# Kernel optimization log

Hardware: AMD Instinct MI355X
Metric: run time of the kernel (lower is better)

## Reference

```python
import jax, jax.numpy as jnp
import numpy as np

GROUP_SIZE = 128
TOP_K = 2
ZERO_POINT = 8  # Marlin symmetric zero point: w = scale * (q - 8)


def _dequant_int4(q, scales, group_size):
    # q: [E, N, K] int values in [0,15]; scales: [E, N, K//group_size]
    s = jnp.repeat(scales, group_size, axis=-1)  # [E, N, K]
    return (q.astype(jnp.float32) - float(ZERO_POINT)) * s


def setup_inputs() -> dict:
    key = jax.random.key(0)
    k1, k2, k3, k4, k5, k6 = jax.random.split(key, 6)
    B, S, H, I, E = 2, 1024, 2048, 1408, 8
    router_logits = jax.random.normal(k1, (B, S, E), dtype=jnp.float32)
    hidden_states = jax.random.normal(k2, (B, S, H), dtype=jnp.float32)
    fc_gate_up_qweights = jax.random.randint(k3, (E, 2 * I, H), 0, 16, dtype=jnp.int32)
    fc_gate_up_scales = jax.random.uniform(k4, (E, 2 * I, H // GROUP_SIZE), dtype=jnp.float32) * 0.02
    fc_down_qweights = jax.random.randint(k5, (E, H, I), 0, 16, dtype=jnp.int32)
    fc_down_scales = jax.random.uniform(k6, (E, H, I // GROUP_SIZE), dtype=jnp.float32) * 0.02
    return {
        "router_logits": router_logits,
        "hidden_states": hidden_states,
        "fc_gate_up_qweights": fc_gate_up_qweights,
        "fc_gate_up_scales": fc_gate_up_scales,
        "fc_down_qweights": fc_down_qweights,
        "fc_down_scales": fc_down_scales,
    }


def reference(router_logits, hidden_states, fc_gate_up_qweights, fc_gate_up_scales,
              fc_down_qweights, fc_down_scales):
    B, S, H = hidden_states.shape
    E = router_logits.shape[-1]
    T = B * S
    x = hidden_states.reshape(T, H)
    logits = router_logits.reshape(T, E)

    # top-k routing with softmax over selected logits
    top_vals, top_idx = jax.lax.top_k(logits, TOP_K)          # [T, k]
    top_w = jax.nn.softmax(top_vals, axis=-1)                 # [T, k]
    route_w = jnp.zeros((T, E), x.dtype).at[jnp.arange(T)[:, None], top_idx].set(top_w)  # [T, E]

    # dequantize int4 weights: scale * (q - 8), per-group along K
    w_gate_up = _dequant_int4(fc_gate_up_qweights, fc_gate_up_scales, GROUP_SIZE)  # [E, 2I, H]
    w_down = _dequant_int4(fc_down_qweights, fc_down_scales, GROUP_SIZE)          # [E, H, I]

    # grouped GEMM (dense over experts, masked by routing weights)
    gu = jnp.einsum('th,enh->ten', x, w_gate_up)              # [T, E, 2I]
    gate, up = jnp.split(gu, 2, axis=-1)
    act = jax.nn.silu(gate) * up                              # SwiGLU, [T, E, I]
    out = jnp.einsum('tei,ehi,te->th', act, w_down, route_w)  # [T, H]
    return out.reshape(B, S, H)
```

## Files before the change

kernel.cpp:

```cpp
#include <hip/hip_runtime.h>
#include <hip/hip_bf16.h>

#define T_TOKENS 2048
#define H_DIM    2048
#define I_DIM    1408
#define E_NUM    8

typedef __bf16 bf16;
typedef __attribute__((ext_vector_type(8))) __bf16  bf16x8;
typedef __attribute__((ext_vector_type(4))) float   floatx4;

static const size_t OFF_COUNTS = 0;
static const size_t OFF_LISTS  = 256;
static const size_t OFF_WLISTS = OFF_LISTS + (size_t)T_TOKENS * E_NUM * 4;
static const size_t OFF_XB     = 131328;
static const size_t OFF_ACT    = OFF_XB + (size_t)T_TOKENS * H_DIM * 2;
static const size_t OFF_GUPK   = OFF_ACT + (size_t)2 * T_TOKENS * I_DIM * 2;
static const size_t OFF_DNPK   = OFF_GUPK + (size_t)E_NUM * 22 * 32 * 16384;
static const size_t OFF_TMP    = OFF_GUPK;

__device__ __forceinline__ void gload_lds16(const bf16* g, bf16* l)
{
    __builtin_amdgcn_global_load_lds((const __attribute__((address_space(1))) void*)g,
                                     (__attribute__((address_space(3))) void*)l,
                                     16, 0, 0);
}

__global__ __launch_bounds__(256) void prep_kernel(
    const int*   __restrict__ gu_q,
    const float* __restrict__ gu_s,
    bf16*        __restrict__ gu_pk,
    const float* __restrict__ x,
    bf16*        __restrict__ xb,
    const float* __restrict__ logits,
    int*         __restrict__ counts,
    int*         __restrict__ lists,
    float*       __restrict__ wlists)
{
    const int bid = blockIdx.x;
    const int tid = threadIdx.x;

    if (bid < 5632) {
        const int kt  = bid & 31;
        const int en  = bid >> 5;
        const int nt  = en % 22;
        const int e   = en / 22;
        bf16x8* ob = reinterpret_cast<bf16x8*>(gu_pk) + (size_t)bid * 1024;
        #pragma unroll
        for (int j = 0; j < 4; ++j) {
            const int s     = tid + 256 * j;
            const int r     = s >> 3;
            const int gl    = (s & 7) ^ (r & 7);
            const int p2    = r >> 4;
            const int is_up = p2 & 1;
            const int icol  = nt * 64 + (p2 >> 1) * 16 + (r & 15);
            const size_t row_q = (size_t)e * 2816 + (is_up ? I_DIM : 0) + icol;
            const int4* qp = reinterpret_cast<const int4*>(gu_q + row_q * H_DIM + kt * 64 + gl * 8);
            int4 a = qp[0], c = qp[1];
            float sv = gu_s[row_q * 16 + (kt >> 1)];
            float m8 = -8.f * sv;
            bf16x8 bv;
            bv[0] = (bf16)fmaf((float)a.x, sv, m8);
            bv[1] = (bf16)fmaf((float)a.y, sv, m8);
            bv[2] = (bf16)fmaf((float)a.z, sv, m8);
            bv[3] = (bf16)fmaf((float)a.w, sv, m8);
            bv[4] = (bf16)fmaf((float)c.x, sv, m8);
            bv[5] = (bf16)fmaf((float)c.y, sv, m8);
            bv[6] = (bf16)fmaf((float)c.z, sv, m8);
            bv[7] = (bf16)fmaf((float)c.w, sv, m8);
            ob[s] = bv;
        }
    } else if (bid < 5632 + 2048) {
        const int i = (bid - 5632) * 256 + tid;
        const float4* x4 = reinterpret_cast<const float4*>(x) + (size_t)i * 2;
        float4 v0 = x4[0], v1 = x4[1];
        bf16x8 bv;
        bv[0] = (bf16)v0.x; bv[1] = (bf16)v0.y; bv[2] = (bf16)v0.z; bv[3] = (bf16)v0.w;
        bv[4] = (bf16)v1.x; bv[5] = (bf16)v1.y; bv[6] = (bf16)v1.z; bv[7] = (bf16)v1.w;
        *reinterpret_cast<bf16x8*>(xb + (size_t)i * 8) = bv;
    } else {
        const int t = (bid - 7680) * 256 + tid;
        const float* l = logits + (size_t)t * E_NUM;
        float v0 = -1e30f, v1 = -1e30f;
        int i0 = 0, i1 = 0;
        #pragma unroll
        for (int e = 0; e < E_NUM; ++e) {
            float v = l[e];
            if (v > v0) { v1 = v0; i1 = i0; v0 = v; i0 = e; }
            else if (v > v1) { v1 = v; i1 = e; }
        }
        float w0 = 1.f / (1.f + __expf(v1 - v0));
        float w1 = 1.f - w0;
        int p0 = atomicAdd(&counts[i0], 1);
        lists[i0 * T_TOKENS + p0] = t * 2 + 0;
        wlists[i0 * T_TOKENS + p0] = w0;
        int p1 = atomicAdd(&counts[i1], 1);
        lists[i1 * T_TOKENS + p1] = t * 2 + 1;
        wlists[i1 * T_TOKENS + p1] = w1;
    }
}

__global__ __launch_bounds__(256) void gemm1_packdn_kernel(
    const bf16*  __restrict__ xb,
    const bf16*  __restrict__ wpk,
    const int*   __restrict__ counts,
    const int*   __restrict__ lists,
    bf16*        __restrict__ act,
    const int*   __restrict__ dn_q,
    const float* __restrict__ dn_s,
    bf16*        __restrict__ dn_pk)
{
    const int tid = threadIdx.x;

    if (blockIdx.x >= 5632) {
        const int pbid = blockIdx.x - 5632;
        const int kt  = pbid % 22;
        const int en  = pbid / 22;
        const int nt  = en & 15;
        const int e   = en >> 4;
        bf16x8* ob = reinterpret_cast<bf16x8*>(dn_pk) + (size_t)pbid * 1024;
        #pragma unroll
        for (int j = 0; j < 4; ++j) {
            const int s  = tid + 256 * j;
            const int r  = s >> 3;
            const int gl = (s & 7) ^ (r & 7);
            const size_t row_q = (size_t)e * 2048 + nt * 128 + r;
            const int4* qp = reinterpret_cast<const int4*>(dn_q + row_q * I_DIM + kt * 64 + gl * 8);
            int4 a = qp[0], c = qp[1];
            float sv = dn_s[row_q * 11 + (kt >> 1)];
            float m8 = -8.f * sv;
            bf16x8 bv;
            bv[0] = (bf16)fmaf((float)a.x, sv, m8);
            bv[1] = (bf16)fmaf((float)a.y, sv, m8);
            bv[2] = (bf16)fmaf((float)a.z, sv, m8);
            bv[3] = (bf16)fmaf((float)a.w, sv, m8);
            bv[4] = (bf16)fmaf((float)c.x, sv, m8);
            bv[5] = (bf16)fmaf((float)c.y, sv, m8);
            bv[6] = (bf16)fmaf((float)c.z, sv, m8);
            bv[7] = (bf16)fmaf((float)c.w, sv, m8);
            ob[s] = bv;
        }
        return;
    }

    const int lid = (blockIdx.x & 7) * 704 + (blockIdx.x >> 3);
    const int e   = lid / 704;
    const int r_  = lid - e * 704;
    const int nt  = r_ >> 5;
    const int m0  = (r_ & 31) << 6;
    const int cnt = counts[e];
    if (m0 >= cnt) return;

    __shared__ __align__(16) bf16 Al[4096];
    __shared__ __align__(16) bf16 Bl[8192];
    __shared__ int meta[64];

    if (tid < 64) {
        int m = m0 + tid;
        meta[tid] = lists[e * T_TOKENS + (m < cnt ? m : 0)];
    }
    __syncthreads();

    const int lane = tid & 63;
    const int wv = tid >> 6;
    const int wm = wv >> 1, wn = wv & 1;

    size_t agbl[2];
    #pragma unroll
    for (int j = 0; j < 2; ++j) {
        int g = tid + 256 * j;
        int arow = g >> 3, cg = g & 7;
        agbl[j] = (size_t)(meta[arow] >> 1) * H_DIM + ((cg ^ (arow & 7)) * 8);
    }
    const bf16* bt = wpk + ((size_t)e * 22 + nt) * (32 * 8192) + tid * 8;

    int afr[2][2], bfr[2][4];
    #pragma unroll
    for (int ks = 0; ks < 2; ++ks) {
        int gidx = ks * 4 + (lane >> 4);
        #pragma unroll
        for (int t4 = 0; t4 < 2; ++t4) {
            int ra = wm * 32 + t4 * 16 + (lane & 15);
            afr[ks][t4] = ra * 64 + ((gidx ^ (ra & 7)) * 8);
        }
        #pragma unroll
        for (int t4 = 0; t4 < 4; ++t4) {
            int rb = wn * 64 + t4 * 16 + (lane & 15);
            bfr[ks][t4] = rb * 64 + ((gidx ^ (rb & 7)) * 8);
        }
    }

    floatx4 acc[2][4];
    #pragma unroll
    for (int i = 0; i < 2; ++i)
        #pragma unroll
        for (int j = 0; j < 4; ++j)
            acc[i][j] = (floatx4){0.f, 0.f, 0.f, 0.f};

    for (int k0 = 0; k0 < H_DIM; k0 += 64) {
        #pragma unroll
        for (int j = 0; j < 2; ++j)
            gload_lds16(xb + agbl[j] + k0, &Al[(tid + 256 * j) * 8]);
        const bf16* bsrc = bt + (size_t)(k0 >> 6) * 8192;
        #pragma unroll
        for (int j = 0; j < 4; ++j)
            gload_lds16(bsrc + j * 2048, &Bl[tid * 8 + j * 2048]);
        __syncthreads();
        #pragma unroll
        for (int ks = 0; ks < 2; ++ks) {
            bf16x8 af[2], bff[4];
            #pragma unroll
            for (int mt = 0; mt < 2; ++mt)
                af[mt] = *reinterpret_cast<const bf16x8*>(&Al[afr[ks][mt]]);
            #pragma unroll
            for (int ntf = 0; ntf < 4; ++ntf)
                bff[ntf] = *reinterpret_cast<const bf16x8*>(&Bl[bfr[ks][ntf]]);
            #pragma unroll
            for (int mt = 0; mt < 2; ++mt)
                #pragma unroll
                for (int ntf = 0; ntf < 4; ++ntf)
                    acc[mt][ntf] = __builtin_amdgcn_mfma_f32_16x16x32_bf16(af[mt], bff[ntf], acc[mt][ntf], 0, 0, 0);
        }
        __syncthreads();
    }

    const int rbase = (lane >> 4) * 4;
    const int cn = lane & 15;
    #pragma unroll
    for (int mt = 0; mt < 2; ++mt) {
        #pragma unroll
        for (int j = 0; j < 2; ++j) {
            floatx4 g = acc[mt][2 * j];
            floatx4 u = acc[mt][2 * j + 1];
            int col = nt * 64 + (wn * 2 + j) * 16 + cn;
            #pragma unroll
            for (int r = 0; r < 4; ++r) {
                int lrow = wm * 32 + mt * 16 + rbase + r;
                if (m0 + lrow < cnt) {
                    float gate = g[r], up = u[r];
                    float a = gate / (1.f + __expf(-gate)) * up;
                    act[(size_t)meta[lrow] * I_DIM + col] = (bf16)a;
                }
            }
        }
    }
}

__global__ __launch_bounds__(256) void gemm2_kernel(
    const bf16*  __restrict__ act,
    const bf16*  __restrict__ wpk,
    const int*   __restrict__ counts,
    const int*   __restrict__ lists,
    const float* __restrict__ wlists,
    float*       __restrict__ tmp)
{
    const int lid = (blockIdx.x & 7) * 512 + (blockIdx.x >> 3);
    const int e   = lid >> 9;
    const int r_  = lid & 511;
    const int nt  = r_ >> 5;
    const int m0  = (r_ & 31) << 6;
    const int cnt = counts[e];
    if (m0 >= cnt) return;

    __shared__ __align__(16) bf16 Al[4096];
    __shared__ __align__(16) bf16 Bl[8192];
    __shared__ int   meta[64];
    __shared__ float wmeta[64];

    const int tid = threadIdx.x;
    if (tid < 64) {
        int m = m0 + tid;
        int mm = (m < cnt) ? m : 0;
        meta[tid]  = lists[e * T_TOKENS + mm];
        wmeta[tid] = wlists[e * T_TOKENS + mm];
    }
    __syncthreads();

    const int lane = tid & 63;
    const int wv = tid >> 6;
    const int wm = wv >> 1, wn = wv & 1;

    size_t agbl[2];
    #pragma unroll
    for (int j = 0; j < 2; ++j) {
        int g = tid + 256 * j;
        int arow = g >> 3, cg = g & 7;
        agbl[j] = (size_t)meta[arow] * I_DIM + ((cg ^ (arow & 7)) * 8);
    }
    const bf16* bt = wpk + ((size_t)e * 16 + nt) * (22 * 8192) + tid * 8;

    int afr[2][2], bfr[2][4];
    #pragma unroll
    for (int ks = 0; ks < 2; ++ks) {
        int gidx = ks * 4 + (lane >> 4);
        #pragma unroll
        for (int t4 = 0; t4 < 2; ++t4) {
            int ra = wm * 32 + t4 * 16 + (lane & 15);
            afr[ks][t4] = ra * 64 + ((gidx ^ (ra & 7)) * 8);
        }
        #pragma unroll
        for (int t4 = 0; t4 < 4; ++t4) {
            int rb = wn * 64 + t4 * 16 + (lane & 15);
            bfr[ks][t4] = rb * 64 + ((gidx ^ (rb & 7)) * 8);
        }
    }

    floatx4 acc[2][4];
    #pragma unroll
    for (int i = 0; i < 2; ++i)
        #pragma unroll
        for (int j = 0; j < 4; ++j)
            acc[i][j] = (floatx4){0.f, 0.f, 0.f, 0.f};

    for (int kt = 0; kt < 22; ++kt) {
        #pragma unroll
        for (int j = 0; j < 2; ++j)
            gload_lds16(act + agbl[j] + kt * 64, &Al[(tid + 256 * j) * 8]);
        const bf16* bsrc = bt + (size_t)kt * 8192;
        #pragma unroll
        for (int j = 0; j < 4; ++j)
            gload_lds16(bsrc + j * 2048, &Bl[tid * 8 + j * 2048]);
        __syncthreads();
        #pragma unroll
        for (int ks = 0; ks < 2; ++ks) {
            bf16x8 af[2], bff[4];
            #pragma unroll
            for (int mt = 0; mt < 2; ++mt)
                af[mt] = *reinterpret_cast<const bf16x8*>(&Al[afr[ks][mt]]);
            #pragma unroll
            for (int ntf = 0; ntf < 4; ++ntf)
                bff[ntf] = *reinterpret_cast<const bf16x8*>(&Bl[bfr[ks][ntf]]);
            #pragma unroll
            for (int mt = 0; mt < 2; ++mt)
                #pragma unroll
                for (int ntf = 0; ntf < 4; ++ntf)
                    acc[mt][ntf] = __builtin_amdgcn_mfma_f32_16x16x32_bf16(af[mt], bff[ntf], acc[mt][ntf], 0, 0, 0);
        }
        __syncthreads();
    }

    const int rbase = (lane >> 4) * 4;
    const int cn = lane & 15;
    #pragma unroll
    for (int mt = 0; mt < 2; ++mt) {
        #pragma unroll
        for (int ntf = 0; ntf < 4; ++ntf) {
            floatx4 v = acc[mt][ntf];
            int col = nt * 128 + wn * 64 + ntf * 16 + cn;
            #pragma unroll
            for (int r = 0; r < 4; ++r) {
                int lrow = wm * 32 + mt * 16 + rbase + r;
                if (m0 + lrow < cnt) {
                    tmp[(size_t)meta[lrow] * H_DIM + col] = wmeta[lrow] * v[r];
                }
            }
        }
    }
}

__global__ void finalize_kernel(const float* __restrict__ tmp, float* __restrict__ out)
{
    int i4 = blockIdx.x * blockDim.x + threadIdx.x;
    int t  = i4 >> 9;
    int h  = (i4 & 511) * 4;
    float4 a = *reinterpret_cast<const float4*>(tmp + ((size_t)2 * t) * H_DIM + h);
    float4 b = *reinterpret_cast<const float4*>(tmp + ((size_t)(2 * t + 1)) * H_DIM + h);
    float4 o;
    o.x = a.x + b.x; o.y = a.y + b.y; o.z = a.z + b.z; o.w = a.w + b.w;
    *reinterpret_cast<float4*>(out + (size_t)t * H_DIM + h) = o;
}

extern "C" void kernel_launch(void* const* d_in, const int* in_sizes, int n_in,
                              void* d_out, int out_size, void* d_ws, size_t ws_size,
                              hipStream_t stream)
{
    const float* router_logits = (const float*)d_in[0];
    const float* x             = (const float*)d_in[1];
    const int*   gu_q          = (const int*)d_in[2];
    const float* gu_s          = (const float*)d_in[3];
    const int*   dn_q          = (const int*)d_in[4];
    const float* dn_s          = (const float*)d_in[5];
    float* out = (float*)d_out;

    char* ws = (char*)d_ws;
    int*   counts = (int*)(ws + OFF_COUNTS);
    int*   lists  = (int*)(ws + OFF_LISTS);
    float* wlists = (float*)(ws + OFF_WLISTS);
    bf16*  xb     = (bf16*)(ws + OFF_XB);
    bf16*  act    = (bf16*)(ws + OFF_ACT);
    bf16*  gu_pk  = (bf16*)(ws + OFF_GUPK);
    bf16*  dn_pk  = (bf16*)(ws + OFF_DNPK);
    float* tmp    = (float*)(ws + OFF_TMP);

    hipMemsetAsync(counts, 0, E_NUM * sizeof(int), stream);

    prep_kernel<<<7688, 256, 0, stream>>>(gu_q, gu_s, gu_pk, x, xb,
                                          router_logits, counts, lists, wlists);
    gemm1_packdn_kernel<<<8448, 256, 0, stream>>>(xb, gu_pk, counts, lists, act,
                                                  dn_q, dn_s, dn_pk);
    gemm2_kernel<<<4096, 256, 0, stream>>>(act, dn_pk, counts, lists, wlists, tmp);
    finalize_kernel<<<4096, 256, 0, stream>>>(tmp, out);
}
```

Baseline: 489.0 us.

## Load A operand fragments directly from global memory instead of staging in LDS

Both grouped GEMM kernels drop the LDS staging buffer for the gathered activation (A) tile and have each lane load its MFMA A fragment straight from global memory via per-row base pointers. This removes the A-side LDS writes and reads and halves the LDS footprint, which may allow higher occupancy. In exchange, each A element is now read from global/L2 by both N-waves (wn=0,1) instead of once per block, and the loads are issued after the barrier inside the compute loop, so their latency is exposed right before the MFMAs.

```diff
diff --git a/kernel.cpp b/kernel.cpp
--- a/kernel.cpp
+++ b/kernel.cpp
@@ -151,7 +151,6 @@
     const int cnt = counts[e];
     if (m0 >= cnt) return;
 
-    __shared__ __align__(16) bf16 Al[4096];
     __shared__ __align__(16) bf16 Bl[8192];
     __shared__ int meta[64];
 
@@ -165,24 +164,19 @@
     const int wv = tid >> 6;
     const int wm = wv >> 1, wn = wv & 1;
 
-    size_t agbl[2];
-    #pragma unroll
-    for (int j = 0; j < 2; ++j) {
-        int g = tid + 256 * j;
-        int arow = g >> 3, cg = g & 7;
-        agbl[j] = (size_t)(meta[arow] >> 1) * H_DIM + ((cg ^ (arow & 7)) * 8);
-    }
+    const bf16* abase[2];
+    #pragma unroll
+    for (int mt = 0; mt < 2; ++mt) {
+        int ra = wm * 32 + mt * 16 + (lane & 15);
+        abase[mt] = xb + (size_t)(meta[ra] >> 1) * H_DIM + ((lane >> 4) * 8);
+    }
+
     const bf16* bt = wpk + ((size_t)e * 22 + nt) * (32 * 8192) + tid * 8;
 
-    int afr[2][2], bfr[2][4];
+    int bfr[2][4];
     #pragma unroll
     for (int ks = 0; ks < 2; ++ks) {
         int gidx = ks * 4 + (lane >> 4);
-        #pragma unroll
-        for (int t4 = 0; t4 < 2; ++t4) {
-            int ra = wm * 32 + t4 * 16 + (lane & 15);
-            afr[ks][t4] = ra * 64 + ((gidx ^ (ra & 7)) * 8);
-        }
         #pragma unroll
         for (int t4 = 0; t4 < 4; ++t4) {
             int rb = wn * 64 + t4 * 16 + (lane & 15);
@@ -198,9 +192,6 @@
             acc[i][j] = (floatx4){0.f, 0.f, 0.f, 0.f};
 
     for (int k0 = 0; k0 < H_DIM; k0 += 64) {
-        #pragma unroll
-        for (int j = 0; j < 2; ++j)
-            gload_lds16(xb + agbl[j] + k0, &Al[(tid + 256 * j) * 8]);
         const bf16* bsrc = bt + (size_t)(k0 >> 6) * 8192;
         #pragma unroll
         for (int j = 0; j < 4; ++j)
@@ -211,7 +202,7 @@
             bf16x8 af[2], bff[4];
             #pragma unroll
             for (int mt = 0; mt < 2; ++mt)
-                af[mt] = *reinterpret_cast<const bf16x8*>(&Al[afr[ks][mt]]);
+                af[mt] = *reinterpret_cast<const bf16x8*>(abase[mt] + k0 + ks * 32);
             #pragma unroll
             for (int ntf = 0; ntf < 4; ++ntf)
                 bff[ntf] = *reinterpret_cast<const bf16x8*>(&Bl[bfr[ks][ntf]]);
@@ -262,7 +253,6 @@
     const int cnt = counts[e];
     if (m0 >= cnt) return;
 
-    __shared__ __align__(16) bf16 Al[4096];
     __shared__ __align__(16) bf16 Bl[8192];
     __shared__ int   meta[64];
     __shared__ float wmeta[64];
@@ -280,24 +270,19 @@
     const int wv = tid >> 6;
     const int wm = wv >> 1, wn = wv & 1;
 
-    size_t agbl[2];
-    #pragma unroll
-    for (int j = 0; j < 2; ++j) {
-        int g = tid + 256 * j;
-        int arow = g >> 3, cg = g & 7;
-        agbl[j] = (size_t)meta[arow] * I_DIM + ((cg ^ (arow & 7)) * 8);
-    }
+    const bf16* abase[2];
+    #pragma unroll
+    for (int mt = 0; mt < 2; ++mt) {
+        int ra = wm * 32 + mt * 16 + (lane & 15);
+        abase[mt] = act + (size_t)meta[ra] * I_DIM + ((lane >> 4) * 8);
+    }
+
     const bf16* bt = wpk + ((size_t)e * 16 + nt) * (22 * 8192) + tid * 8;
 
-    int afr[2][2], bfr[2][4];
+    int bfr[2][4];
     #pragma unroll
     for (int ks = 0; ks < 2; ++ks) {
         int gidx = ks * 4 + (lane >> 4);
-        #pragma unroll
-        for (int t4 = 0; t4 < 2; ++t4) {
-            int ra = wm * 32 + t4 * 16 + (lane & 15);
-            afr[ks][t4] = ra * 64 + ((gidx ^ (ra & 7)) * 8);
-        }
         #pragma unroll
         for (int t4 = 0; t4 < 4; ++t4) {
             int rb = wn * 64 + t4 * 16 + (lane & 15);
@@ -313,9 +298,6 @@
             acc[i][j] = (floatx4){0.f, 0.f, 0.f, 0.f};
 
     for (int kt = 0; kt < 22; ++kt) {
-        #pragma unroll
-        for (int j = 0; j < 2; ++j)
-            gload_lds16(act + agbl[j] + kt * 64, &Al[(tid + 256 * j) * 8]);
         const bf16* bsrc = bt + (size_t)kt * 8192;
         #pragma unroll
         for (int j = 0; j < 4; ++j)
@@ -326,7 +308,7 @@
             bf16x8 af[2], bff[4];
             #pragma unroll
             for (int mt = 0; mt < 2; ++mt)
-                af[mt] = *reinterpret_cast<const bf16x8*>(&Al[afr[ks][mt]]);
+                af[mt] = *reinterpret_cast<const bf16x8*>(abase[mt] + kt * 64 + ks * 32);
             #pragma unroll
             for (int ntf = 0; ntf < 4; ++ntf)
                 bff[ntf] = *reinterpret_cast<const bf16x8*>(&Bl[bfr[ks][ntf]]);
```

After: 605.9 us. 1.24x slower.

## Double-buffer LDS tiles in both MoE GEMMs with async prefetch

Applied to the files above, without the earlier changes.

Both grouped GEMM kernels now use two LDS buffers for the A and B tiles and issue global-to-LDS loads for the next K tile before computing on the current one. Partial vmcnt waits plus raw barriers with sched_barrier replace __syncthreads, so the wait covers only the current tile's loads. This aims to hide global memory latency behind MFMA work. In exchange it doubles LDS usage per block, which may lower occupancy, and it relies on a hand-written vmcnt count.

```diff
diff --git a/kernel.cpp b/kernel.cpp
--- a/kernel.cpp
+++ b/kernel.cpp
@@ -25,6 +25,10 @@
                                      (__attribute__((address_space(3))) void*)l,
                                      16, 0, 0);
 }
+
+#define RAW_BAR() do { __builtin_amdgcn_sched_barrier(0); \
+                       __builtin_amdgcn_s_barrier(); \
+                       __builtin_amdgcn_sched_barrier(0); } while (0)
 
 __global__ __launch_bounds__(256) void prep_kernel(
     const int*   __restrict__ gu_q,
@@ -151,8 +155,8 @@
     const int cnt = counts[e];
     if (m0 >= cnt) return;
 
-    __shared__ __align__(16) bf16 Al[4096];
-    __shared__ __align__(16) bf16 Bl[8192];
+    __shared__ __align__(16) bf16 Al[2][4096];
+    __shared__ __align__(16) bf16 Bl[2][8192];
     __shared__ int meta[64];
 
     if (tid < 64) {
@@ -197,31 +201,46 @@
         for (int j = 0; j < 4; ++j)
             acc[i][j] = (floatx4){0.f, 0.f, 0.f, 0.f};
 
-    for (int k0 = 0; k0 < H_DIM; k0 += 64) {
-        #pragma unroll
-        for (int j = 0; j < 2; ++j)
-            gload_lds16(xb + agbl[j] + k0, &Al[(tid + 256 * j) * 8]);
-        const bf16* bsrc = bt + (size_t)(k0 >> 6) * 8192;
-        #pragma unroll
-        for (int j = 0; j < 4; ++j)
-            gload_lds16(bsrc + j * 2048, &Bl[tid * 8 + j * 2048]);
-        __syncthreads();
+    #pragma unroll
+    for (int j = 0; j < 2; ++j)
+        gload_lds16(xb + agbl[j], &Al[0][(tid + 256 * j) * 8]);
+    #pragma unroll
+    for (int j = 0; j < 4; ++j)
+        gload_lds16(bt + j * 2048, &Bl[0][tid * 8 + j * 2048]);
+
+    for (int kt = 0; kt < 32; ++kt) {
+        const int cur = kt & 1;
+        if (kt < 31) {
+            const int k1 = (kt + 1) * 64;
+            #pragma unroll
+            for (int j = 0; j < 2; ++j)
+                gload_lds16(xb + agbl[j] + k1, &Al[cur ^ 1][(tid + 256 * j) * 8]);
+            const bf16* bsrc = bt + (size_t)(kt + 1) * 8192;
+            #pragma unroll
+            for (int j = 0; j < 4; ++j)
+                gload_lds16(bsrc + j * 2048, &Bl[cur ^ 1][tid * 8 + j * 2048]);
+            asm volatile("s_waitcnt vmcnt(6)" ::: "memory");
+        } else {
+            asm volatile("s_waitcnt vmcnt(0)" ::: "memory");
+        }
+        RAW_BAR();
+
         #pragma unroll
         for (int ks = 0; ks < 2; ++ks) {
             bf16x8 af[2], bff[4];
             #pragma unroll
             for (int mt = 0; mt < 2; ++mt)
-                af[mt] = *reinterpret_cast<const bf16x8*>(&Al[afr[ks][mt]]);
+                af[mt] = *reinterpret_cast<const bf16x8*>(&Al[cur][afr[ks][mt]]);
             #pragma unroll
             for (int ntf = 0; ntf < 4; ++ntf)
-                bff[ntf] = *reinterpret_cast<const bf16x8*>(&Bl[bfr[ks][ntf]]);
+                bff[ntf] = *reinterpret_cast<const bf16x8*>(&Bl[cur][bfr[ks][ntf]]);
             #pragma unroll
             for (int mt = 0; mt < 2; ++mt)
                 #pragma unroll
                 for (int ntf = 0; ntf < 4; ++ntf)
                     acc[mt][ntf] = __builtin_amdgcn_mfma_f32_16x16x32_bf16(af[mt], bff[ntf], acc[mt][ntf], 0, 0, 0);
         }
-        __syncthreads();
+        RAW_BAR();
     }
 
     const int rbase = (lane >> 4) * 4;
@@ -262,8 +281,8 @@
     const int cnt = counts[e];
     if (m0 >= cnt) return;
 
-    __shared__ __align__(16) bf16 Al[4096];
-    __shared__ __align__(16) bf16 Bl[8192];
+    __shared__ __align__(16) bf16 Al[2][4096];
+    __shared__ __align__(16) bf16 Bl[2][8192];
     __shared__ int   meta[64];
     __shared__ float wmeta[64];
 
@@ -312,31 +331,46 @@
         for (int j = 0; j < 4; ++j)
             acc[i][j] = (floatx4){0.f, 0.f, 0.f, 0.f};
 
+    #pragma unroll
+    for (int j = 0; j < 2; ++j)
+        gload_lds16(act + agbl[j], &Al[0][(tid + 256 * j) * 8]);
+    #pragma unroll
+    for (int j = 0; j < 4; ++j)
+        gload_lds16(bt + j * 2048, &Bl[0][tid * 8 + j * 2048]);
+
     for (int kt = 0; kt < 22; ++kt) {
-        #pragma unroll
-        for (int j = 0; j < 2; ++j)
-            gload_lds16(act + agbl[j] + kt * 64, &Al[(tid + 256 * j) * 8]);
-        const bf16* bsrc = bt + (size_t)kt * 8192;
-        #pragma unroll
-        for (int j = 0; j < 4; ++j)
-            gload_lds16(bsrc + j * 2048, &Bl[tid * 8 + j * 2048]);
-        __syncthreads();
+        const int cur = kt & 1;
+        if (kt < 21) {
+            const int k1 = (kt + 1) * 64;
+            #pragma unroll
+            for (int j = 0; j < 2; ++j)
+                gload_lds16(act + agbl[j] + k1, &Al[cur ^ 1][(tid + 256 * j) * 8]);
+            const bf16* bsrc = bt + (size_t)(kt + 1) * 8192;
+            #pragma unroll
+            for (int j = 0; j < 4; ++j)
+                gload_lds16(bsrc + j * 2048, &Bl[cur ^ 1][tid * 8 + j * 2048]);
+            asm volatile("s_waitcnt vmcnt(6)" ::: "memory");
+        } else {
+            asm volatile("s_waitcnt vmcnt(0)" ::: "memory");
+        }
+        RAW_BAR();
+
         #pragma unroll
         for (int ks = 0; ks < 2; ++ks) {
             bf16x8 af[2], bff[4];
             #pragma unroll
             for (int mt = 0; mt < 2; ++mt)
-                af[mt] = *reinterpret_cast<const bf16x8*>(&Al[afr[ks][mt]]);
+                af[mt] = *reinterpret_cast<const bf16x8*>(&Al[cur][afr[ks][mt]]);
             #pragma unroll
             for (int ntf = 0; ntf < 4; ++ntf)
-                bff[ntf] = *reinterpret_cast<const bf16x8*>(&Bl[bfr[ks][ntf]]);
+                bff[ntf] = *reinterpret_cast<const bf16x8*>(&Bl[cur][bfr[ks][ntf]]);
             #pragma unroll
             for (int mt = 0; mt < 2; ++mt)
                 #pragma unroll
                 for (int ntf = 0; ntf < 4; ++ntf)
                     acc[mt][ntf] = __builtin_amdgcn_mfma_f32_16x16x32_bf16(af[mt], bff[ntf], acc[mt][ntf], 0, 0, 0);
         }
-        __syncthreads();
+        RAW_BAR();
     }
 
     const int rbase = (lane >> 4) * 4;
```

New measurement: 511.6 us. 4.6% more time.

## Fuse int4 weight dequantization into GEMM tile loads, dropping the pre-pack passes

Applied to the files above, without the earlier changes.

Removes the separate passes that dequantized gate/up and down weights into packed bf16 buffers, and instead has each GEMM block read int32 quantized weights and scales directly, dequantize in registers, and store to LDS. This eliminates the pack writes and the workspace buffers. In exchange, every m-tile re-reads the 4-byte-per-element quantized weights and repeats the conversion math, and B loads become synchronous register loads instead of direct-to-LDS loads.

```diff
diff --git a/kernel.cpp b/kernel.cpp
--- a/kernel.cpp
+++ b/kernel.cpp
@@ -15,9 +15,7 @@
 static const size_t OFF_WLISTS = OFF_LISTS + (size_t)T_TOKENS * E_NUM * 4;
 static const size_t OFF_XB     = 131328;
 static const size_t OFF_ACT    = OFF_XB + (size_t)T_TOKENS * H_DIM * 2;
-static const size_t OFF_GUPK   = OFF_ACT + (size_t)2 * T_TOKENS * I_DIM * 2;
-static const size_t OFF_DNPK   = OFF_GUPK + (size_t)E_NUM * 22 * 32 * 16384;
-static const size_t OFF_TMP    = OFF_GUPK;
+static const size_t OFF_TMP    = OFF_ACT + (size_t)2 * T_TOKENS * I_DIM * 2;
 
 __device__ __forceinline__ void gload_lds16(const bf16* g, bf16* l)
 {
@@ -27,9 +25,6 @@
 }
 
 __global__ __launch_bounds__(256) void prep_kernel(
-    const int*   __restrict__ gu_q,
-    const float* __restrict__ gu_s,
-    bf16*        __restrict__ gu_pk,
     const float* __restrict__ x,
     bf16*        __restrict__ xb,
     const float* __restrict__ logits,
@@ -40,38 +35,8 @@
     const int bid = blockIdx.x;
     const int tid = threadIdx.x;
 
-    if (bid < 5632) {
-        const int kt  = bid & 31;
-        const int en  = bid >> 5;
-        const int nt  = en % 22;
-        const int e   = en / 22;
-        bf16x8* ob = reinterpret_cast<bf16x8*>(gu_pk) + (size_t)bid * 1024;
-        #pragma unroll
-        for (int j = 0; j < 4; ++j) {
-            const int s     = tid + 256 * j;
-            const int r     = s >> 3;
-            const int gl    = (s & 7) ^ (r & 7);
-            const int p2    = r >> 4;
-            const int is_up = p2 & 1;
-            const int icol  = nt * 64 + (p2 >> 1) * 16 + (r & 15);
-            const size_t row_q = (size_t)e * 2816 + (is_up ? I_DIM : 0) + icol;
-            const int4* qp = reinterpret_cast<const int4*>(gu_q + row_q * H_DIM + kt * 64 + gl * 8);
-            int4 a = qp[0], c = qp[1];
-            float sv = gu_s[row_q * 16 + (kt >> 1)];
-            float m8 = -8.f * sv;
-            bf16x8 bv;
-            bv[0] = (bf16)fmaf((float)a.x, sv, m8);
-            bv[1] = (bf16)fmaf((float)a.y, sv, m8);
-            bv[2] = (bf16)fmaf((float)a.z, sv, m8);
-            bv[3] = (bf16)fmaf((float)a.w, sv, m8);
-            bv[4] = (bf16)fmaf((float)c.x, sv, m8);
-            bv[5] = (bf16)fmaf((float)c.y, sv, m8);
-            bv[6] = (bf16)fmaf((float)c.z, sv, m8);
-            bv[7] = (bf16)fmaf((float)c.w, sv, m8);
-            ob[s] = bv;
-        }
-    } else if (bid < 5632 + 2048) {
-        const int i = (bid - 5632) * 256 + tid;
+    if (bid < 2048) {
+        const int i = bid * 256 + tid;
         const float4* x4 = reinterpret_cast<const float4*>(x) + (size_t)i * 2;
         float4 v0 = x4[0], v1 = x4[1];
         bf16x8 bv;
@@ -79,7 +44,7 @@
         bv[4] = (bf16)v1.x; bv[5] = (bf16)v1.y; bv[6] = (bf16)v1.z; bv[7] = (bf16)v1.w;
         *reinterpret_cast<bf16x8*>(xb + (size_t)i * 8) = bv;
     } else {
-        const int t = (bid - 7680) * 256 + tid;
+        const int t = (bid - 2048) * 256 + tid;
         const float* l = logits + (size_t)t * E_NUM;
         float v0 = -1e30f, v1 = -1e30f;
         int i0 = 0, i1 = 0;
@@ -100,49 +65,14 @@
     }
 }
 
-__global__ __launch_bounds__(256) void gemm1_packdn_kernel(
+__global__ __launch_bounds__(256) void gemm1_kernel(
     const bf16*  __restrict__ xb,
-    const bf16*  __restrict__ wpk,
+    const int*   __restrict__ q,
+    const float* __restrict__ sc,
     const int*   __restrict__ counts,
     const int*   __restrict__ lists,
-    bf16*        __restrict__ act,
-    const int*   __restrict__ dn_q,
-    const float* __restrict__ dn_s,
-    bf16*        __restrict__ dn_pk)
-{
-    const int tid = threadIdx.x;
-
-    if (blockIdx.x >= 5632) {
-        const int pbid = blockIdx.x - 5632;
-        const int kt  = pbid % 22;
-        const int en  = pbid / 22;
-        const int nt  = en & 15;
-        const int e   = en >> 4;
-        bf16x8* ob = reinterpret_cast<bf16x8*>(dn_pk) + (size_t)pbid * 1024;
-        #pragma unroll
-        for (int j = 0; j < 4; ++j) {
-            const int s  = tid + 256 * j;
-            const int r  = s >> 3;
-            const int gl = (s & 7) ^ (r & 7);
-            const size_t row_q = (size_t)e * 2048 + nt * 128 + r;
-            const int4* qp = reinterpret_cast<const int4*>(dn_q + row_q * I_DIM + kt * 64 + gl * 8);
-            int4 a = qp[0], c = qp[1];
-            float sv = dn_s[row_q * 11 + (kt >> 1)];
-            float m8 = -8.f * sv;
-            bf16x8 bv;
-            bv[0] = (bf16)fmaf((float)a.x, sv, m8);
-            bv[1] = (bf16)fmaf((float)a.y, sv, m8);
-            bv[2] = (bf16)fmaf((float)a.z, sv, m8);
-            bv[3] = (bf16)fmaf((float)a.w, sv, m8);
-            bv[4] = (bf16)fmaf((float)c.x, sv, m8);
-            bv[5] = (bf16)fmaf((float)c.y, sv, m8);
-            bv[6] = (bf16)fmaf((float)c.z, sv, m8);
-            bv[7] = (bf16)fmaf((float)c.w, sv, m8);
-            ob[s] = bv;
-        }
-        return;
-    }
-
+    bf16*        __restrict__ act)
+{
     const int lid = (blockIdx.x & 7) * 704 + (blockIdx.x >> 3);
     const int e   = lid / 704;
     const int r_  = lid - e * 704;
@@ -155,6 +85,7 @@
     __shared__ __align__(16) bf16 Bl[8192];
     __shared__ int meta[64];
 
+    const int tid = threadIdx.x;
     if (tid < 64) {
         int m = m0 + tid;
         meta[tid] = lists[e * T_TOKENS + (m < cnt ? m : 0)];
@@ -172,7 +103,20 @@
         int arow = g >> 3, cg = g & 7;
         agbl[j] = (size_t)(meta[arow] >> 1) * H_DIM + ((cg ^ (arow & 7)) * 8);
     }
-    const bf16* bt = wpk + ((size_t)e * 22 + nt) * (32 * 8192) + tid * 8;
+
+    const int gl = (tid & 7) ^ ((tid >> 3) & 7);
+    const int*   qb_[4];
+    const float* sb_[4];
+    #pragma unroll
+    for (int j = 0; j < 4; ++j) {
+        int r     = (tid >> 3) + 32 * j;
+        int p2    = r >> 4;
+        int is_up = p2 & 1;
+        int icol  = nt * 64 + (p2 >> 1) * 16 + (r & 15);
+        size_t row_q = (size_t)e * 2816 + (is_up ? I_DIM : 0) + icol;
+        qb_[j] = q  + row_q * H_DIM + gl * 8;
+        sb_[j] = sc + row_q * 16;
+    }
 
     int afr[2][2], bfr[2][4];
     #pragma unroll
@@ -197,14 +141,28 @@
         for (int j = 0; j < 4; ++j)
             acc[i][j] = (floatx4){0.f, 0.f, 0.f, 0.f};
 
-    for (int k0 = 0; k0 < H_DIM; k0 += 64) {
+    for (int kt = 0; kt < 32; ++kt) {
+        const int k0 = kt * 64;
         #pragma unroll
         for (int j = 0; j < 2; ++j)
             gload_lds16(xb + agbl[j] + k0, &Al[(tid + 256 * j) * 8]);
-        const bf16* bsrc = bt + (size_t)(k0 >> 6) * 8192;
-        #pragma unroll
-        for (int j = 0; j < 4; ++j)
-            gload_lds16(bsrc + j * 2048, &Bl[tid * 8 + j * 2048]);
+        #pragma unroll
+        for (int j = 0; j < 4; ++j) {
+            const int4* p = reinterpret_cast<const int4*>(qb_[j] + k0);
+            int4 a = p[0], c = p[1];
+            float s = sb_[j][kt >> 1];
+            float m8 = -8.f * s;
+            bf16x8 bv;
+            bv[0] = (bf16)fmaf((float)a.x, s, m8);
+            bv[1] = (bf16)fmaf((float)a.y, s, m8);
+            bv[2] = (bf16)fmaf((float)a.z, s, m8);
+            bv[3] = (bf16)fmaf((float)a.w, s, m8);
+            bv[4] = (bf16)fmaf((float)c.x, s, m8);
+            bv[5] = (bf16)fmaf((float)c.y, s, m8);
+            bv[6] = (bf16)fmaf((float)c.z, s, m8);
+            bv[7] = (bf16)fmaf((float)c.w, s, m8);
+            *reinterpret_cast<bf16x8*>(&Bl[(tid + 256 * j) * 8]) = bv;
+        }
         __syncthreads();
         #pragma unroll
         for (int ks = 0; ks < 2; ++ks) {
@@ -248,7 +206,8 @@
 
 __global__ __launch_bounds__(256) void gemm2_kernel(
     const bf16*  __restrict__ act,
-    const bf16*  __restrict__ wpk,
+    const int*   __restrict__ q,
+    const float* __restrict__ sc,
     const int*   __restrict__ counts,
     const int*   __restrict__ lists,
     const float* __restrict__ wlists,
@@ -287,7 +246,17 @@
         int arow = g >> 3, cg = g & 7;
         agbl[j] = (size_t)meta[arow] * I_DIM + ((cg ^ (arow & 7)) * 8);
     }
-    const bf16* bt = wpk + ((size_t)e * 16 + nt) * (22 * 8192) + tid * 8;
+
+    const int gl = (tid & 7) ^ ((tid >> 3) & 7);
+    const int*   qb_[4];
+    const float* sb_[4];
+    #pragma unroll
+    for (int j = 0; j < 4; ++j) {
+        int r = (tid >> 3) + 32 * j;
+        size_t row_q = (size_t)e * 2048 + nt * 128 + r;
+        qb_[j] = q  + row_q * I_DIM + gl * 8;
+        sb_[j] = sc + row_q * 11;
+    }
 
     int afr[2][2], bfr[2][4];
     #pragma unroll
@@ -313,13 +282,27 @@
             acc[i][j] = (floatx4){0.f, 0.f, 0.f, 0.f};
 
     for (int kt = 0; kt < 22; ++kt) {
+        const int k0 = kt * 64;
         #pragma unroll
         for (int j = 0; j < 2; ++j)
-            gload_lds16(act + agbl[j] + kt * 64, &Al[(tid + 256 * j) * 8]);
-        const bf16* bsrc = bt + (size_t)kt * 8192;
-        #pragma unroll
-        for (int j = 0; j < 4; ++j)
-            gload_lds16(bsrc + j * 2048, &Bl[tid * 8 + j * 2048]);
+            gload_lds16(act + agbl[j] + k0, &Al[(tid + 256 * j) * 8]);
+        #pragma unroll
+        for (int j = 0; j < 4; ++j) {
+            const int4* p = reinterpret_cast<const int4*>(qb_[j] + k0);
+            int4 a = p[0], c = p[1];
+            float s = sb_[j][kt >> 1];
+            float m8 = -8.f * s;
+            bf16x8 bv;
+            bv[0] = (bf16)fmaf((float)a.x, s, m8);
+            bv[1] = (bf16)fmaf((float)a.y, s, m8);
+            bv[2] = (bf16)fmaf((float)a.z, s, m8);
+            bv[3] = (bf16)fmaf((float)a.w, s, m8);
+            bv[4] = (bf16)fmaf((float)c.x, s, m8);
+            bv[5] = (bf16)fmaf((float)c.y, s, m8);
+            bv[6] = (bf16)fmaf((float)c.z, s, m8);
+            bv[7] = (bf16)fmaf((float)c.w, s, m8);
+            *reinterpret_cast<bf16x8*>(&Bl[(tid + 256 * j) * 8]) = bv;
+        }
         __syncthreads();
         #pragma unroll
         for (int ks = 0; ks < 2; ++ks) {
@@ -388,16 +371,12 @@
     float* wlists = (float*)(ws + OFF_WLISTS);
     bf16*  xb     = (bf16*)(ws + OFF_XB);
     bf16*  act    = (bf16*)(ws + OFF_ACT);
-    bf16*  gu_pk  = (bf16*)(ws + OFF_GUPK);
-    bf16*  dn_pk  = (bf16*)(ws + OFF_DNPK);
     float* tmp    = (float*)(ws + OFF_TMP);
 
     hipMemsetAsync(counts, 0, E_NUM * sizeof(int), stream);
 
-    prep_kernel<<<7688, 256, 0, stream>>>(gu_q, gu_s, gu_pk, x, xb,
-                                          router_logits, counts, lists, wlists);
-    gemm1_packdn_kernel<<<8448, 256, 0, stream>>>(xb, gu_pk, counts, lists, act,
-                                                  dn_q, dn_s, dn_pk);
-    gemm2_kernel<<<4096, 256, 0, stream>>>(act, dn_pk, counts, lists, wlists, tmp);
+    prep_kernel<<<2056, 256, 0, stream>>>(x, xb, router_logits, counts, lists, wlists);
+    gemm1_kernel<<<5632, 256, 0, stream>>>(xb, gu_q, gu_s, counts, lists, act);
+    gemm2_kernel<<<4096, 256, 0, stream>>>(act, dn_q, dn_s, counts, lists, wlists, tmp);
     finalize_kernel<<<4096, 256, 0, stream>>>(tmp, out);
 }
```

Result: slower. 546.7 us (+11.8%).
